# Kernel optimization log

Measured on AMD Instinct MI355X. Metric: run time of the kernel, lower is better.

The kernel has to match this reference:

```python
import jax, jax.numpy as jnp
import numpy as np

N_NODES = 50000
N_EDGES = 800000


def gat_conv(x, src, dst, ea, W, We, a_s, a_d, a_e, b, n_nodes):
    """PyG GATConv with edge_dim, add_self_loops=True, fill_value='mean', concat=True."""
    H, C = a_s.shape
    dt = x.dtype
    # self-loop edge_attr = mean of incoming edge attrs per destination node
    deg = jax.ops.segment_sum(jnp.ones((src.shape[0],), dt), dst, num_segments=n_nodes)
    loop_attr = jax.ops.segment_sum(ea, dst, num_segments=n_nodes) / jnp.clip(deg, 1.0)[:, None]
    nodes = jnp.arange(n_nodes, dtype=src.dtype)
    s = jnp.concatenate([src, nodes])
    d = jnp.concatenate([dst, nodes])
    e_attr = jnp.concatenate([ea, loop_attr], axis=0)       # [E2, edge_dim]
    h = (x @ W).reshape(n_nodes, H, C)                       # [N,H,C]
    e = (e_attr @ We).reshape(-1, H, C)                      # [E2,H,C]
    a_src = jnp.einsum('nhc,hc->nh', h, a_s)                 # [N,H]
    a_dst = jnp.einsum('nhc,hc->nh', h, a_d)
    a_edg = jnp.einsum('ehc,hc->eh', e, a_e)                 # [E2,H]
    lg = jax.nn.leaky_relu(a_src[s] + a_dst[d] + a_edg, 0.2)  # [E2,H]
    m = jax.ops.segment_max(lg, d, num_segments=n_nodes)     # every node has a self-loop
    p = jnp.exp(lg - m[d])
    z = jax.ops.segment_sum(p, d, num_segments=n_nodes)
    alpha = p / z[d]                                         # segment softmax over dst
    out = jax.ops.segment_sum(alpha[:, :, None] * h[s], d, num_segments=n_nodes)
    return out.reshape(n_nodes, H * C) + b


def setup_inputs() -> dict:
    key = jax.random.key(0)
    ks = iter(jax.random.split(key, 40))
    sc = 0.05
    inp = {
        'x': jax.random.normal(next(ks), (N_NODES, 128), jnp.float32),
        'edge_index': jax.random.randint(next(ks), (2, N_EDGES), 0, N_NODES, dtype=jnp.int32),
        'edge_attr': jax.random.uniform(next(ks), (N_EDGES, 1), jnp.float32),
        'fa_w': jax.random.normal(next(ks), (128, 128)) * sc, 'fa_b': jnp.zeros((128,)),
        'W1': jax.random.normal(next(ks), (128, 256)) * sc, 'We1': jax.random.normal(next(ks), (1, 256)) * sc,
        'as1': jax.random.normal(next(ks), (4, 64)) * sc, 'ad1': jax.random.normal(next(ks), (4, 64)) * sc,
        'ae1': jax.random.normal(next(ks), (4, 64)) * sc, 'b1': jnp.zeros((256,)),
        'W2': jax.random.normal(next(ks), (256, 256)) * sc, 'We2': jax.random.normal(next(ks), (1, 256)) * sc,
        'as2': jax.random.normal(next(ks), (4, 64)) * sc, 'ad2': jax.random.normal(next(ks), (4, 64)) * sc,
        'ae2': jax.random.normal(next(ks), (4, 64)) * sc, 'b2': jnp.zeros((256,)),
        'W3': jax.random.normal(next(ks), (256, 64)) * sc, 'We3': jax.random.normal(next(ks), (1, 64)) * sc,
        'as3': jax.random.normal(next(ks), (1, 64)) * sc, 'ad3': jax.random.normal(next(ks), (1, 64)) * sc,
        'ae3': jax.random.normal(next(ks), (1, 64)) * sc, 'b3': jnp.zeros((64,)),
        'r1_w': jax.random.normal(next(ks), (128, 256)) * sc, 'r1_b': jnp.zeros((256,)),
        'r2_w': jax.random.normal(next(ks), (256, 256)) * sc, 'r2_b': jnp.zeros((256,)),
        'ffn_w1': jax.random.normal(next(ks), (128, 64)) * sc, 'ffn_b1': jnp.zeros((64,)),
        'ffn_w2': jax.random.normal(next(ks), (64, 64)) * sc, 'ffn_b2': jnp.zeros((64,)),
    }
    return inp


def reference(x, edge_index, edge_attr, fa_w, fa_b,
              W1, We1, as1, ad1, ae1, b1,
              W2, We2, as2, ad2, ae2, b2,
              W3, We3, as3, ad3, ae3, b3,
              r1_w, r1_b, r2_w, r2_b,
              ffn_w1, ffn_b1, ffn_w2, ffn_b2):
    n = x.shape[0]
    src, dst = edge_index[0], edge_index[1]
    # feature attention gate
    x = x * jax.nn.sigmoid(x @ fa_w + fa_b)
    xr1 = x @ r1_w + r1_b
    z1 = gat_conv(x, src, dst, edge_attr, W1, We1, as1, ad1, ae1, b1, n)
    z1 = jax.nn.leaky_relu(z1, 0.01) + xr1          # dropout = identity (eval)
    z2 = gat_conv(z1, src, dst, edge_attr, W2, We2, as2, ad2, ae2, b2, n)
    z2 = jax.nn.leaky_relu(z2, 0.01) + (z1 @ r2_w + r2_b)
    z3 = gat_conv(z2, src, dst, edge_attr, W3, We3, as3, ad3, ae3, b3, n)
    z_self = jax.nn.relu(x @ ffn_w1 + ffn_b1) @ ffn_w2 + ffn_b2
    z3 = jax.nn.leaky_relu(z3, 0.01) + z_self
    return z3
```

## Files before the change

### kernel.cpp

```cpp
#include <hip/hip_runtime.h>
#include <hip/hip_bf16.h>


typedef unsigned short u16;
typedef unsigned int   u32;
typedef __attribute__((ext_vector_type(8))) short short8;
typedef __attribute__((ext_vector_type(4))) float float4v;

typedef const __attribute__((address_space(1))) u32* gptr_t;
typedef __attribute__((address_space(3))) u32* lptr_t;
#define GLOAD_LDS16(g, l) \
    __builtin_amdgcn_global_load_lds((gptr_t)(const void*)(g), (lptr_t)(void*)(l), 16, 0, 0)

static __device__ __forceinline__ u16 f2b(float f) {
    u32 u = __float_as_uint(f);
    u32 r = u + 0x7fffu + ((u >> 16) & 1u);
    return (u16)(r >> 16);
}
static __device__ __forceinline__ float b2f(u16 u) {
    return __uint_as_float(((u32)u) << 16);
}
static __device__ __forceinline__ float lo2f(u32 v) { return __uint_as_float(v << 16); }
static __device__ __forceinline__ float hi2f(u32 v) { return __uint_as_float(v & 0xffff0000u); }
static __device__ __forceinline__ float lrelu02(float x) { return fmaxf(x, 0.2f * x); }

__global__ void prep_mega(const float* __restrict__ x, u16* __restrict__ xb, int n4,
                          const float* s0, const float* s1, const float* s2,
                          const float* s3, const float* s4, const float* s5,
                          const float* s6, const float* s7,
                          u16* d0, u16* d1, u16* d2, u16* d3,
                          u16* d4, u16* d5, u16* d6, u16* d7,
                          const float* We1, const float* ae1,
                          const float* We2, const float* ae2,
                          const float* We3, const float* ae3, float* ce_g,
                          const int* __restrict__ ei,
                          u32* deg, u32* rank, int E) {
    int role = blockIdx.y;
    if (role == 0) {
        int i = blockIdx.x * 256 + threadIdx.x;
        if (i >= n4) return;
        float4 v = ((const float4*)x)[i];
        ushort4 o;
        o.x = f2b(v.x); o.y = f2b(v.y); o.z = f2b(v.z); o.w = f2b(v.w);
        ((ushort4*)xb)[i] = o;
    } else if (role == 2) {
        int e = blockIdx.x * 256 + threadIdx.x;
        if (e >= E) return;
        int d = ei[E + e];
        rank[e] = atomicAdd(&deg[d], 1u);
    } else {
        int wid = blockIdx.x >> 4, sub = blockIdx.x & 15;
        if (wid > 8) return;
        if (wid == 8) {
            if (sub == 0) {
                int t = threadIdx.x;
                if (t < 9) {
                    const float* W; const float* a; int h;
                    if (t < 4)      { W = We1; a = ae1; h = t; }
                    else if (t < 8) { W = We2; a = ae2; h = t - 4; }
                    else            { W = We3; a = ae3; h = 0; }
                    float s = 0.f;
                    for (int c = 0; c < 64; c++) s += W[h * 64 + c] * a[h * 64 + c];
                    ce_g[t] = s;
                }
            }
            return;
        }
        const float* src; u16* dst; int K, N;
        switch (wid) {
            case 0: src = s0; dst = d0; K = 128; N = 128; break;
            case 1: src = s1; dst = d1; K = 128; N = 256; break;
            case 2: src = s2; dst = d2; K = 128; N = 256; break;
            case 3: src = s3; dst = d3; K = 256; N = 256; break;
            case 4: src = s4; dst = d4; K = 256; N = 256; break;
            case 5: src = s5; dst = d5; K = 256; N = 64;  break;
            case 6: src = s6; dst = d6; K = 128; N = 64;  break;
            default: src = s7; dst = d7; K = 64;  N = 64;  break;
        }
        int KN = K * N;
        int nmask = N - 1;
        int nshift = __popc((u32)nmask);
        for (int i = sub * 256 + threadIdx.x; i < KN; i += 16 * 256) {
            int k = i >> nshift, n2 = i & nmask;
            dst[(size_t)n2 * K + k] = f2b(src[i]);
        }
    }
}

__global__ void scan_block_kernel(const u32* __restrict__ deg, int* incl,
                                  int* blocksum, int Nn) {
    __shared__ int sb[256];
    int t = threadIdx.x;
    int n = blockIdx.x * 256 + t;
    int v = (n < Nn) ? (int)deg[n] : 0;
    sb[t] = v;
    __syncthreads();
    for (int off = 1; off < 256; off <<= 1) {
        int x = (t >= off) ? sb[t - off] : 0;
        __syncthreads();
        sb[t] += x;
        __syncthreads();
    }
    if (n < Nn) incl[n] = sb[t];
    if (t == 255) blocksum[blockIdx.x] = sb[255];
}

__global__ void scan_final_kernel(const u32* __restrict__ deg, const int* __restrict__ incl,
                                  const int* __restrict__ blocksum,
                                  int* row_ptr, int Nn) {
    __shared__ int sb[256];
    int t = threadIdx.x;
    int b = blockIdx.x;
    sb[t] = (t < b) ? blocksum[t] : 0;
    __syncthreads();
    for (int off = 128; off > 0; off >>= 1) {
        if (t < off) sb[t] += sb[t + off];
        __syncthreads();
    }
    int base = sb[0];
    int n = b * 256 + t;
    if (n >= Nn) return;
    int d = (int)deg[n];
    int excl = base + incl[n] - d;
    row_ptr[n] = excl;
    if (n == Nn - 1) row_ptr[Nn] = excl + d;
}

__global__ void scatter_kernel(const int* __restrict__ ei, const float* __restrict__ ea,
                               const int* __restrict__ row_ptr, const u32* __restrict__ rank,
                               int2* __restrict__ csr2, int E) {
    int e = blockIdx.x * 256 + threadIdx.x;
    if (e >= E) return;
    int d = ei[E + e];
    int pos = row_ptr[d] + (int)rank[e];
    csr2[pos] = make_int2(ei[e], __float_as_int(ea[e]));
}

template <int EPI, int K>
__global__ __launch_bounds__(256)
void gemm128_kernel(const u16* __restrict__ A, const u16* __restrict__ Bt,
                    const float* __restrict__ bias,
                    float* __restrict__ Cf, u16* __restrict__ Cb, int N) {
    __shared__ u16 As[128 * 32];
    __shared__ u16 Bs[128 * 32];
    int t = threadIdx.x;
    int w = t >> 6, lane = t & 63;
    int wm = w & 1, wn = w >> 1;
    int lm = lane & 15, q = lane >> 4;
    int bm = blockIdx.x * 128, bn = blockIdx.y * 128;

    float4v acc[4][4];
#pragma unroll
    for (int i = 0; i < 4; i++)
#pragma unroll
        for (int j = 0; j < 4; j++) acc[i][j] = (float4v){0.f, 0.f, 0.f, 0.f};

    int srow = lane >> 2;
    int scol = (lane & 3) * 8;
    const u16* aG = A + (size_t)(bm + w * 32 + srow) * K + scol;
    const u16* bG = Bt + (size_t)(bn + w * 32 + srow) * K + scol;
    u16* aL0 = &As[(w * 32) * 32];
    u16* aL1 = &As[(w * 32 + 16) * 32];
    u16* bL0 = &Bs[(w * 32) * 32];
    u16* bL1 = &Bs[(w * 32 + 16) * 32];

#pragma unroll
    for (int k0 = 0; k0 < K; k0 += 32) {
        GLOAD_LDS16(aG + k0, aL0);
        GLOAD_LDS16(aG + (size_t)16 * K + k0, aL1);
        GLOAD_LDS16(bG + k0, bL0);
        GLOAD_LDS16(bG + (size_t)16 * K + k0, bL1);
        __syncthreads();

        short8 af[4], bf[4];
#pragma unroll
        for (int i = 0; i < 4; i++)
            af[i] = *(const short8*)&As[(64 * wm + 16 * i + lm) * 32 + q * 8];
#pragma unroll
        for (int j = 0; j < 4; j++)
            bf[j] = *(const short8*)&Bs[(64 * wn + 16 * j + lm) * 32 + q * 8];
#pragma unroll
        for (int i = 0; i < 4; i++)
#pragma unroll
            for (int j = 0; j < 4; j++)
                acc[i][j] = __builtin_amdgcn_mfma_f32_16x16x32_bf16(af[i], bf[j], acc[i][j], 0, 0, 0);
        __syncthreads();
    }

#pragma unroll
    for (int i = 0; i < 4; i++)
#pragma unroll
        for (int j = 0; j < 4; j++) {
            int col = bn + 64 * wn + 16 * j + lm;
#pragma unroll
            for (int r = 0; r < 4; r++) {
                int row = bm + 64 * wm + 16 * i + q * 4 + r;
                float v = acc[i][j][r];
                if (EPI == 4) {
                    if (col < 256) {
                        v += bias[col];
                        Cf[(size_t)row * 256 + col] = v;
                    } else {
                        Cb[(size_t)row * 256 + (col - 256)] = f2b(v);
                    }
                } else {
                    Cb[(size_t)row * N + col] = f2b(v);
                }
            }
        }
}

template <int EPI, int K>
__global__ __launch_bounds__(256)
void gemm_kernel(const u16* __restrict__ A, const u16* __restrict__ Bt,
                 const float* __restrict__ bias, const u16* __restrict__ extraB,
                 float* __restrict__ Cf, u16* __restrict__ Cb, int N) {
#define LDSS 40
    __shared__ u16 As[64 * LDSS];
    __shared__ u16 Bs[64 * LDSS];
    int t = threadIdx.x;
    int bm = blockIdx.x * 64, bn = blockIdx.y * 64;
    int w = t >> 6, lane = t & 63;
    int wm = w & 1, wn = w >> 1;
    int lm = lane & 15, q = lane >> 4;

    float4v acc[2][2];
#pragma unroll
    for (int i = 0; i < 2; i++)
#pragma unroll
        for (int j = 0; j < 2; j++) acc[i][j] = (float4v){0.f, 0.f, 0.f, 0.f};

    int ar = t >> 2;
    int ac = (t & 3) * 8;
    const u16* aPtr = A + (size_t)(bm + ar) * K + ac;
    const u16* bPtr = Bt + (size_t)(bn + ar) * K + ac;

#pragma unroll
    for (int k0 = 0; k0 < K; k0 += 32) {
        uint4 av = *(const uint4*)(aPtr + k0);
        uint4 bv = *(const uint4*)(bPtr + k0);
        *(uint4*)&As[ar * LDSS + ac] = av;
        *(uint4*)&Bs[ar * LDSS + ac] = bv;
        __syncthreads();

        short8 fa0 = *(const short8*)&As[(32 * wm + lm) * LDSS + q * 8];
        short8 fa1 = *(const short8*)&As[(32 * wm + 16 + lm) * LDSS + q * 8];
        short8 fb0 = *(const short8*)&Bs[(32 * wn + lm) * LDSS + q * 8];
        short8 fb1 = *(const short8*)&Bs[(32 * wn + 16 + lm) * LDSS + q * 8];
        acc[0][0] = __builtin_amdgcn_mfma_f32_16x16x32_bf16(fa0, fb0, acc[0][0], 0, 0, 0);
        acc[0][1] = __builtin_amdgcn_mfma_f32_16x16x32_bf16(fa0, fb1, acc[0][1], 0, 0, 0);
        acc[1][0] = __builtin_amdgcn_mfma_f32_16x16x32_bf16(fa1, fb0, acc[1][0], 0, 0, 0);
        acc[1][1] = __builtin_amdgcn_mfma_f32_16x16x32_bf16(fa1, fb1, acc[1][1], 0, 0, 0);
        __syncthreads();
    }

#pragma unroll
    for (int i = 0; i < 2; i++)
#pragma unroll
        for (int j = 0; j < 2; j++) {
            int col = bn + 32 * wn + 16 * j + lm;
            float bval = (EPI >= 1) ? bias[col] : 0.f;
#pragma unroll
            for (int r = 0; r < 4; r++) {
                int row = bm + 32 * wm + 16 * i + q * 4 + r;
                float v = acc[i][j][r] + bval;
                if (EPI == 2) v = fmaxf(v, 0.f);
                if (EPI == 3) {
                    float xv = b2f(extraB[(size_t)row * N + col]);
                    v = xv / (1.f + __expf(-v));
                }
                size_t o = (size_t)row * N + col;
                if (EPI == 1) Cf[o] = v;
                else Cb[o] = f2b(v);
            }
        }
}

__global__ __launch_bounds__(256)
void att4_kernel(const uint2* __restrict__ hb2, const float* __restrict__ a_s,
                 const float* __restrict__ a_d, float* att_s, float* att_d, int Nn) {
    int wv = threadIdx.x >> 6;
    int n = blockIdx.x * 4 + wv;
    if (n >= Nn) return;
    int lane = threadIdx.x & 63;
    float4 as4 = *(const float4*)&a_s[lane * 4];
    float4 ad4 = *(const float4*)&a_d[lane * 4];
    uint2 v = hb2[(size_t)n * 64 + lane];
    float c0 = lo2f(v.x), c1 = hi2f(v.x), c2 = lo2f(v.y), c3 = hi2f(v.y);
    float ps = c0 * as4.x + c1 * as4.y + c2 * as4.z + c3 * as4.w;
    float pd = c0 * ad4.x + c1 * ad4.y + c2 * ad4.z + c3 * ad4.w;
#pragma unroll
    for (int off = 8; off > 0; off >>= 1) {
        ps += __shfl_down(ps, off);
        pd += __shfl_down(pd, off);
    }
    if ((lane & 15) == 0) {
        att_s[n * 4 + (lane >> 4)] = ps;
        att_d[n * 4 + (lane >> 4)] = pd;
    }
}

__global__ __launch_bounds__(256)
void att1_kernel(const u32* __restrict__ hb, const float* __restrict__ a_s,
                 const float* __restrict__ a_d, float* att_s, float* att_d, int Nn) {
    int wv = threadIdx.x >> 6;
    int n = blockIdx.x * 4 + wv;
    if (n >= Nn) return;
    int lane = threadIdx.x & 63;
    int cl = lane & 31;
    float2 as2 = *(const float2*)&a_s[cl * 2];
    float2 ad2 = *(const float2*)&a_d[cl * 2];
    u32 v = hb[(u32)n * 32u + cl];
    float c0 = lo2f(v), c1 = hi2f(v);
    float ps = c0 * as2.x + c1 * as2.y;
    float pd = c0 * ad2.x + c1 * ad2.y;
    if (lane >= 32) { ps = 0.f; pd = 0.f; }
#pragma unroll
    for (int off = 16; off > 0; off >>= 1) {
        ps += __shfl_down(ps, off);
        pd += __shfl_down(pd, off);
    }
    if (lane == 0) {
        att_s[n] = ps;
        att_d[n] = pd;
    }
}

__global__ __launch_bounds__(256)
void agg4_kernel(const uint2* __restrict__ hb2,
                 const float* __restrict__ att_s, const float* __restrict__ att_d,
                 const int* __restrict__ row_ptr, const int2* __restrict__ csr2,
                 const float* __restrict__ ce_g, const float* __restrict__ bias,
                 const float* __restrict__ resid, u16* __restrict__ outb, int Nn) {
    int wv = __builtin_amdgcn_readfirstlane(threadIdx.x >> 6);
    int n = blockIdx.x * 4 + wv;
    if (n >= Nn) return;
    int lane = threadIdx.x & 63;
    int hh = lane >> 4;

    float ce = ce_g[hh];
    float adn = att_d[n * 4 + hh];
    float asn = att_s[n * 4 + hh];
    uint2 sv = hb2[(size_t)n * 64 + lane];
    float z = 0.f, qsum = 0.f;
    float aA0 = 0.f, aA1 = 0.f, aA2 = 0.f, aA3 = 0.f;
    float aB0 = 0.f, aB1 = 0.f, aB2 = 0.f, aB3 = 0.f;

    int e0 = row_ptr[n], e1 = row_ptr[n + 1];
    for (int base = e0; base < e1; base += 64) {
        int cnt = min(64, e1 - base);
        int2 cc = csr2[base + min(lane, cnt - 1)];
        int vsrc = cc.x;
        float vea = __int_as_float(cc.y);
        int i = 0;
        for (; i + 8 <= cnt; i += 8) {
            int s0 = __shfl(vsrc, i),     s1 = __shfl(vsrc, i + 1);
            int s2 = __shfl(vsrc, i + 2), s3 = __shfl(vsrc, i + 3);
            int s4 = __shfl(vsrc, i + 4), s5 = __shfl(vsrc, i + 5);
            int s6 = __shfl(vsrc, i + 6), s7 = __shfl(vsrc, i + 7);
            float q0 = __shfl(vea, i),     q1 = __shfl(vea, i + 1);
            float q2 = __shfl(vea, i + 2), q3 = __shfl(vea, i + 3);
            float q4 = __shfl(vea, i + 4), q5 = __shfl(vea, i + 5);
            float q6 = __shfl(vea, i + 6), q7 = __shfl(vea, i + 7);
            float g0 = att_s[(u32)s0 * 4u + hh], g1 = att_s[(u32)s1 * 4u + hh];
            float g2 = att_s[(u32)s2 * 4u + hh], g3 = att_s[(u32)s3 * 4u + hh];
            float g4 = att_s[(u32)s4 * 4u + hh], g5 = att_s[(u32)s5 * 4u + hh];
            float g6 = att_s[(u32)s6 * 4u + hh], g7 = att_s[(u32)s7 * 4u + hh];
            uint2 v0 = hb2[(u32)s0 * 64u + lane], v1 = hb2[(u32)s1 * 64u + lane];
            uint2 v2 = hb2[(u32)s2 * 64u + lane], v3 = hb2[(u32)s3 * 64u + lane];
            uint2 v4 = hb2[(u32)s4 * 64u + lane], v5 = hb2[(u32)s5 * 64u + lane];
            uint2 v6 = hb2[(u32)s6 * 64u + lane], v7 = hb2[(u32)s7 * 64u + lane];
            float p0 = __expf(lrelu02(g0 + adn + q0 * ce));
            float p1 = __expf(lrelu02(g1 + adn + q1 * ce));
            float p2 = __expf(lrelu02(g2 + adn + q2 * ce));
            float p3 = __expf(lrelu02(g3 + adn + q3 * ce));
            float p4 = __expf(lrelu02(g4 + adn + q4 * ce));
            float p5 = __expf(lrelu02(g5 + adn + q5 * ce));
            float p6 = __expf(lrelu02(g6 + adn + q6 * ce));
            float p7 = __expf(lrelu02(g7 + adn + q7 * ce));
            qsum += ((q0 + q1) + (q2 + q3)) + ((q4 + q5) + (q6 + q7));
            z += ((p0 + p1) + (p2 + p3)) + ((p4 + p5) + (p6 + p7));
            aA0 = fmaf(p0, lo2f(v0.x), aA0); aA1 = fmaf(p0, hi2f(v0.x), aA1);
            aA2 = fmaf(p0, lo2f(v0.y), aA2); aA3 = fmaf(p0, hi2f(v0.y), aA3);
            aB0 = fmaf(p1, lo2f(v1.x), aB0); aB1 = fmaf(p1, hi2f(v1.x), aB1);
            aB2 = fmaf(p1, lo2f(v1.y), aB2); aB3 = fmaf(p1, hi2f(v1.y), aB3);
            aA0 = fmaf(p2, lo2f(v2.x), aA0); aA1 = fmaf(p2, hi2f(v2.x), aA1);
            aA2 = fmaf(p2, lo2f(v2.y), aA2); aA3 = fmaf(p2, hi2f(v2.y), aA3);
            aB0 = fmaf(p3, lo2f(v3.x), aB0); aB1 = fmaf(p3, hi2f(v3.x), aB1);
            aB2 = fmaf(p3, lo2f(v3.y), aB2); aB3 = fmaf(p3, hi2f(v3.y), aB3);
            aA0 = fmaf(p4, lo2f(v4.x), aA0); aA1 = fmaf(p4, hi2f(v4.x), aA1);
            aA2 = fmaf(p4, lo2f(v4.y), aA2); aA3 = fmaf(p4, hi2f(v4.y), aA3);
            aB0 = fmaf(p5, lo2f(v5.x), aB0); aB1 = fmaf(p5, hi2f(v5.x), aB1);
            aB2 = fmaf(p5, lo2f(v5.y), aB2); aB3 = fmaf(p5, hi2f(v5.y), aB3);
            aA0 = fmaf(p6, lo2f(v6.x), aA0); aA1 = fmaf(p6, hi2f(v6.x), aA1);
            aA2 = fmaf(p6, lo2f(v6.y), aA2); aA3 = fmaf(p6, hi2f(v6.y), aA3);
            aB0 = fmaf(p7, lo2f(v7.x), aB0); aB1 = fmaf(p7, hi2f(v7.x), aB1);
            aB2 = fmaf(p7, lo2f(v7.y), aB2); aB3 = fmaf(p7, hi2f(v7.y), aB3);
        }
        for (; i < cnt; i++) {
            int s = __shfl(vsrc, i);
            float q = __shfl(vea, i);
            float g = att_s[(u32)s * 4u + hh];
            uint2 v = hb2[(u32)s * 64u + lane];
            float p = __expf(lrelu02(g + adn + q * ce));
            qsum += q;
            z += p;
            aA0 = fmaf(p, lo2f(v.x), aA0); aA1 = fmaf(p, hi2f(v.x), aA1);
            aA2 = fmaf(p, lo2f(v.y), aA2); aA3 = fmaf(p, hi2f(v.y), aA3);
        }
    }
    float la = qsum / (float)max(e1 - e0, 1);
    float ps = __expf(lrelu02(asn + adn + la * ce));
    z += ps;
    float a0 = aA0 + aB0 + ps * lo2f(sv.x);
    float a1 = aA1 + aB1 + ps * hi2f(sv.x);
    float a2 = aA2 + aB2 + ps * lo2f(sv.y);
    float a3 = aA3 + aB3 + ps * hi2f(sv.y);

    float inv = 1.f / z;
    int c0 = lane * 4;
    float4 bv = *(const float4*)&bias[c0];
    float4 rv = *(const float4*)&resid[(size_t)n * 256 + c0];
    float o0 = fmaf(a0, inv, bv.x);
    float o1 = fmaf(a1, inv, bv.y);
    float o2 = fmaf(a2, inv, bv.z);
    float o3 = fmaf(a3, inv, bv.w);
    o0 = fmaxf(o0, 0.01f * o0) + rv.x;
    o1 = fmaxf(o1, 0.01f * o1) + rv.y;
    o2 = fmaxf(o2, 0.01f * o2) + rv.z;
    o3 = fmaxf(o3, 0.01f * o3) + rv.w;
    uint2 packed;
    packed.x = ((u32)f2b(o0)) | (((u32)f2b(o1)) << 16);
    packed.y = ((u32)f2b(o2)) | (((u32)f2b(o3)) << 16);
    ((uint2*)outb)[(size_t)n * 64 + lane] = packed;
}

__global__ __launch_bounds__(256)
void agg1_kernel(const uint2* __restrict__ hb2,
                 const float* __restrict__ att_s, const float* __restrict__ att_d,
                 const int* __restrict__ row_ptr, const int2* __restrict__ csr2,
                 const float* __restrict__ ce_g, const float* __restrict__ bias,
                 const float* __restrict__ resid, float* __restrict__ outf, int Nn) {
    int wv = __builtin_amdgcn_readfirstlane(threadIdx.x >> 6);
    int n = blockIdx.x * 4 + wv;
    if (n >= Nn) return;
    int lane = threadIdx.x & 63;
    int qtr = lane >> 4;
    int cl = lane & 15;

    float ce = ce_g[8];
    float adn = att_d[n];
    float asn = att_s[n];
    uint2 sv = hb2[(u32)n * 16u + cl];
    float z = 0.f, qsum = 0.f;
    float a0 = 0.f, a1 = 0.f, a2 = 0.f, a3 = 0.f;

    int e0 = row_ptr[n], e1 = row_ptr[n + 1];
    for (int base = e0; base < e1; base += 64) {
        int cnt = min(64, e1 - base);
        int2 cc = csr2[base + min(lane, cnt - 1)];
        int vsrc = cc.x;
        float vea = __int_as_float(cc.y);
        for (int i = 0; i < cnt; i += 4) {
            int idx = min(i + qtr, cnt - 1);
            int s = __shfl(vsrc, idx);
            float q = __shfl(vea, idx);
            bool act = (i + qtr < cnt);
            float p = __expf(lrelu02(att_s[s] + adn + q * ce));
            p = act ? p : 0.f;
            q = act ? q : 0.f;
            uint2 v = hb2[(u32)s * 16u + cl];
            z += p;
            qsum += q;
            a0 = fmaf(p, lo2f(v.x), a0);
            a1 = fmaf(p, hi2f(v.x), a1);
            a2 = fmaf(p, lo2f(v.y), a2);
            a3 = fmaf(p, hi2f(v.y), a3);
        }
    }
    z += __shfl_xor(z, 16);      z += __shfl_xor(z, 32);
    qsum += __shfl_xor(qsum, 16); qsum += __shfl_xor(qsum, 32);
    a0 += __shfl_xor(a0, 16);    a0 += __shfl_xor(a0, 32);
    a1 += __shfl_xor(a1, 16);    a1 += __shfl_xor(a1, 32);
    a2 += __shfl_xor(a2, 16);    a2 += __shfl_xor(a2, 32);
    a3 += __shfl_xor(a3, 16);    a3 += __shfl_xor(a3, 32);

    float la = qsum / (float)max(e1 - e0, 1);
    float ps = __expf(lrelu02(asn + adn + la * ce));
    z += ps;
    a0 += ps * lo2f(sv.x);
    a1 += ps * hi2f(sv.x);
    a2 += ps * lo2f(sv.y);
    a3 += ps * hi2f(sv.y);

    if (lane < 16) {
        float inv = 1.f / z;
        int c0 = cl * 4;
        float4 bv = *(const float4*)&bias[c0];
        float4 rv = *(const float4*)&resid[(size_t)n * 64 + c0];
        float o0 = fmaf(a0, inv, bv.x);
        float o1 = fmaf(a1, inv, bv.y);
        float o2 = fmaf(a2, inv, bv.z);
        float o3 = fmaf(a3, inv, bv.w);
        o0 = fmaxf(o0, 0.01f * o0) + rv.x;
        o1 = fmaxf(o1, 0.01f * o1) + rv.y;
        o2 = fmaxf(o2, 0.01f * o2) + rv.z;
        o3 = fmaxf(o3, 0.01f * o3) + rv.w;
        *(float4*)&outf[(size_t)n * 64 + c0] = make_float4(o0, o1, o2, o3);
    }
}

extern "C" void kernel_launch(void* const* d_in, const int* in_sizes, int n_in,
                              void* d_out, int out_size, void* d_ws, size_t ws_size,
                              hipStream_t stream) {
    const float* x    = (const float*)d_in[0];
    const int*   ei   = (const int*)d_in[1];
    const float* ea   = (const float*)d_in[2];
    const float* fa_w = (const float*)d_in[3];
    const float* fa_b = (const float*)d_in[4];
    const float* W1   = (const float*)d_in[5];
    const float* We1  = (const float*)d_in[6];
    const float* as1  = (const float*)d_in[7];
    const float* ad1  = (const float*)d_in[8];
    const float* ae1  = (const float*)d_in[9];
    const float* b1   = (const float*)d_in[10];
    const float* W2   = (const float*)d_in[11];
    const float* We2  = (const float*)d_in[12];
    const float* as2  = (const float*)d_in[13];
    const float* ad2  = (const float*)d_in[14];
    const float* ae2  = (const float*)d_in[15];
    const float* b2   = (const float*)d_in[16];
    const float* W3   = (const float*)d_in[17];
    const float* We3  = (const float*)d_in[18];
    const float* as3  = (const float*)d_in[19];
    const float* ad3  = (const float*)d_in[20];
    const float* ae3  = (const float*)d_in[21];
    const float* b3   = (const float*)d_in[22];
    const float* r1_w = (const float*)d_in[23];
    const float* r1_b = (const float*)d_in[24];
    const float* r2_w = (const float*)d_in[25];
    const float* r2_b = (const float*)d_in[26];
    const float* fw1  = (const float*)d_in[27];
    const float* fb1  = (const float*)d_in[28];
    const float* fw2  = (const float*)d_in[29];
    const float* fb2  = (const float*)d_in[30];

    const int Nn = in_sizes[0] / 128;
    const int E  = in_sizes[1] / 2;

    char* ws = (char*)d_ws;
    size_t off = 0;
    auto alloc = [&](size_t bytes) -> char* {
        char* p = ws + off;
        off += (bytes + 255) & ~((size_t)255);
        return p;
    };
    u32*   deg      = (u32*)alloc((size_t)Nn * 4);
    u32*   rank     = (u32*)alloc((size_t)E * 4);
    int*   incl     = (int*)alloc((size_t)Nn * 4);
    int*   row_ptr  = (int*)alloc((size_t)(Nn + 1) * 4);
    int*   blocksum = (int*)alloc(1024);
    float* att_s    = (float*)alloc((size_t)Nn * 16);
    float* att_d    = (float*)alloc((size_t)Nn * 16);
    int2*  csr2     = (int2*)alloc((size_t)E * 8);
    float* ce_g     = (float*)alloc(64);
    u16* xbf   = (u16*)alloc((size_t)(Nn + 128) * 128 * 2);
    u16* xg_bf = (u16*)alloc((size_t)(Nn + 128) * 128 * 2);
    u16* h_bf  = (u16*)alloc((size_t)(Nn + 128) * 256 * 2);
    u16* z_bf  = (u16*)alloc((size_t)(Nn + 128) * 256 * 2);
    u16* mid_bf = (u16*)alloc((size_t)(Nn + 128) * 64 * 2);
    u16* h3_bf  = (u16*)alloc((size_t)(Nn + 128) * 64 * 2);
    u16* wt_fa = (u16*)alloc(16384 * 2);
    u16* wt_c1 = (u16*)alloc((size_t)512 * 128 * 2);
    u16* wt_c2 = (u16*)alloc((size_t)512 * 256 * 2);
    u16* wt_W3 = (u16*)alloc(16384 * 2);
    u16* wt_f1 = (u16*)alloc(8192 * 2);
    u16* wt_f2 = (u16*)alloc(4096 * 2);
    float* residB = (float*)alloc((size_t)(Nn + 128) * 256 * 4);
    float* zself  = (float*)alloc((size_t)(Nn + 128) * 64 * 4);

    hipMemsetAsync(deg, 0, (size_t)Nn * 4, stream);

    int eb = (E + 255) / 256;
    int nb = (Nn + 255) / 256;
    int n4 = Nn * 128 / 4;
    int xb4 = (n4 + 255) / 256;

    prep_mega<<<dim3(max(xb4, eb), 3), 256, 0, stream>>>(
        x, xbf, n4,
        fa_w, r1_w, W1, r2_w, W2, W3, fw1, fw2,
        wt_fa, wt_c1, wt_c1 + (size_t)256 * 128, wt_c2, wt_c2 + (size_t)256 * 256,
        wt_W3, wt_f1, wt_f2, We1, ae1, We2, ae2, We3, ae3, ce_g,
        ei, deg, rank, E);
    scan_block_kernel<<<nb, 256, 0, stream>>>(deg, incl, blocksum, Nn);
    scan_final_kernel<<<nb, 256, 0, stream>>>(deg, incl, blocksum, row_ptr, Nn);
    scatter_kernel<<<eb, 256, 0, stream>>>(ei, ea, row_ptr, rank, csr2, E);

    int mb  = (Nn + 63) / 64;
    int mb1 = (Nn + 127) / 128;
    int ab  = (Nn + 3) / 4;

    gemm_kernel<3, 128><<<dim3(mb, 2), 256, 0, stream>>>(xbf, wt_fa, fa_b, xbf, nullptr, xg_bf, 128);
    gemm128_kernel<4, 128><<<dim3(mb1, 4), 256, 0, stream>>>(xg_bf, wt_c1, r1_b, residB, h_bf, 512);
    att4_kernel<<<ab, 256, 0, stream>>>((const uint2*)h_bf, as1, ad1, att_s, att_d, Nn);
    agg4_kernel<<<ab, 256, 0, stream>>>((const uint2*)h_bf, att_s, att_d, row_ptr, csr2,
                                        ce_g, b1, residB, z_bf, Nn);
    gemm128_kernel<4, 256><<<dim3(mb1, 4), 256, 0, stream>>>(z_bf, wt_c2, r2_b, residB, h_bf, 512);
    att4_kernel<<<ab, 256, 0, stream>>>((const uint2*)h_bf, as2, ad2, att_s, att_d, Nn);
    agg4_kernel<<<ab, 256, 0, stream>>>((const uint2*)h_bf, att_s, att_d, row_ptr, csr2,
                                        ce_g + 4, b2, residB, z_bf, Nn);
    gemm_kernel<2, 128><<<dim3(mb, 1), 256, 0, stream>>>(xg_bf, wt_f1, fb1, nullptr, nullptr, mid_bf, 64);
    gemm_kernel<1, 64><<<dim3(mb, 1), 256, 0, stream>>>(mid_bf, wt_f2, fb2, nullptr, zself, nullptr, 64);
    gemm_kernel<0, 256><<<dim3(mb, 1), 256, 0, stream>>>(z_bf, wt_W3, nullptr, nullptr, nullptr, h3_bf, 64);
    att1_kernel<<<ab, 256, 0, stream>>>((const u32*)h3_bf, as3, ad3, att_s, att_d, Nn);
    agg1_kernel<<<ab, 256, 0, stream>>>((const uint2*)h3_bf, att_s, att_d, row_ptr, csr2,
                                        ce_g, b3, zself, (float*)d_out, Nn);
}
```

Measured before the change: 490.3 us.

## Fuse FFN first layer into conv1 GEMM, store residuals in bf16, unroll agg by 4

Appends the ffn_w1 weights as an extra 128-column tile to the first combined GEMM, so the ReLU FFN hidden layer is written from its epilogue and its separate launch goes away. Residual and z_self buffers become bf16 instead of fp32, halving their write and read traffic in the GEMM epilogues and aggregation kernels. The agg4 gather loop is unrolled by 4 instead of 8, which lowers register pressure but exposes less memory-level parallelism. The bf16 residuals add rounding error, and the fifth GEMM column tile computes 64 columns that are discarded.

```diff
diff --git a/kernel.cpp b/kernel.cpp
--- a/kernel.cpp
+++ b/kernel.cpp
@@ -139,8 +139,8 @@
 template <int EPI, int K>
 __global__ __launch_bounds__(256)
 void gemm128_kernel(const u16* __restrict__ A, const u16* __restrict__ Bt,
-                    const float* __restrict__ bias,
-                    float* __restrict__ Cf, u16* __restrict__ Cb, int N) {
+                    const float* __restrict__ bias1, const float* __restrict__ bias2,
+                    u16* __restrict__ Cres, u16* __restrict__ Ch, u16* __restrict__ Cmid) {
     __shared__ u16 As[128 * 32];
     __shared__ u16 Bs[128 * 32];
     int t = threadIdx.x;
@@ -196,15 +196,12 @@
             for (int r = 0; r < 4; r++) {
                 int row = bm + 64 * wm + 16 * i + q * 4 + r;
                 float v = acc[i][j][r];
-                if (EPI == 4) {
-                    if (col < 256) {
-                        v += bias[col];
-                        Cf[(size_t)row * 256 + col] = v;
-                    } else {
-                        Cb[(size_t)row * 256 + (col - 256)] = f2b(v);
-                    }
-                } else {
-                    Cb[(size_t)row * N + col] = f2b(v);
+                if (col < 256) {
+                    Cres[(size_t)row * 256 + col] = f2b(v + bias1[col]);
+                } else if (EPI == 4 || col < 512) {
+                    Ch[(size_t)row * 256 + (col - 256)] = f2b(v);
+                } else if (col < 576) {
+                    Cmid[(size_t)row * 64 + (col - 512)] = f2b(fmaxf(v + bias2[col - 512], 0.f));
                 }
             }
         }
@@ -214,7 +211,7 @@
 __global__ __launch_bounds__(256)
 void gemm_kernel(const u16* __restrict__ A, const u16* __restrict__ Bt,
                  const float* __restrict__ bias, const u16* __restrict__ extraB,
-                 float* __restrict__ Cf, u16* __restrict__ Cb, int N) {
+                 u16* __restrict__ Cb, int N) {
 #define LDSS 40
     __shared__ u16 As[64 * LDSS];
     __shared__ u16 Bs[64 * LDSS];
@@ -264,14 +261,11 @@
             for (int r = 0; r < 4; r++) {
                 int row = bm + 32 * wm + 16 * i + q * 4 + r;
                 float v = acc[i][j][r] + bval;
-                if (EPI == 2) v = fmaxf(v, 0.f);
                 if (EPI == 3) {
                     float xv = b2f(extraB[(size_t)row * N + col]);
                     v = xv / (1.f + __expf(-v));
                 }
-                size_t o = (size_t)row * N + col;
-                if (EPI == 1) Cf[o] = v;
-                else Cb[o] = f2b(v);
+                Cb[(size_t)row * N + col] = f2b(v);
             }
         }
 }
@@ -331,7 +325,7 @@
                  const float* __restrict__ att_s, const float* __restrict__ att_d,
                  const int* __restrict__ row_ptr, const int2* __restrict__ csr2,
                  const float* __restrict__ ce_g, const float* __restrict__ bias,
-                 const float* __restrict__ resid, u16* __restrict__ outb, int Nn) {
+                 const uint2* __restrict__ resid2, u16* __restrict__ outb, int Nn) {
     int wv = __builtin_amdgcn_readfirstlane(threadIdx.x >> 6);
     int n = blockIdx.x * 4 + wv;
     if (n >= Nn) return;
@@ -353,49 +347,29 @@
         int vsrc = cc.x;
         float vea = __int_as_float(cc.y);
         int i = 0;
-        for (; i + 8 <= cnt; i += 8) {
-            int s0 = __shfl(vsrc, i),     s1 = __shfl(vsrc, i + 1);
-            int s2 = __shfl(vsrc, i + 2), s3 = __shfl(vsrc, i + 3);
-            int s4 = __shfl(vsrc, i + 4), s5 = __shfl(vsrc, i + 5);
-            int s6 = __shfl(vsrc, i + 6), s7 = __shfl(vsrc, i + 7);
-            float q0 = __shfl(vea, i),     q1 = __shfl(vea, i + 1);
-            float q2 = __shfl(vea, i + 2), q3 = __shfl(vea, i + 3);
-            float q4 = __shfl(vea, i + 4), q5 = __shfl(vea, i + 5);
-            float q6 = __shfl(vea, i + 6), q7 = __shfl(vea, i + 7);
-            float g0 = att_s[(u32)s0 * 4u + hh], g1 = att_s[(u32)s1 * 4u + hh];
-            float g2 = att_s[(u32)s2 * 4u + hh], g3 = att_s[(u32)s3 * 4u + hh];
-            float g4 = att_s[(u32)s4 * 4u + hh], g5 = att_s[(u32)s5 * 4u + hh];
-            float g6 = att_s[(u32)s6 * 4u + hh], g7 = att_s[(u32)s7 * 4u + hh];
-            uint2 v0 = hb2[(u32)s0 * 64u + lane], v1 = hb2[(u32)s1 * 64u + lane];
-            uint2 v2 = hb2[(u32)s2 * 64u + lane], v3 = hb2[(u32)s3 * 64u + lane];
-            uint2 v4 = hb2[(u32)s4 * 64u + lane], v5 = hb2[(u32)s5 * 64u + lane];
-            uint2 v6 = hb2[(u32)s6 * 64u + lane], v7 = hb2[(u32)s7 * 64u + lane];
-            float p0 = __expf(lrelu02(g0 + adn + q0 * ce));
-            float p1 = __expf(lrelu02(g1 + adn + q1 * ce));
-            float p2 = __expf(lrelu02(g2 + adn + q2 * ce));
-            float p3 = __expf(lrelu02(g3 + adn + q3 * ce));
-            float p4 = __expf(lrelu02(g4 + adn + q4 * ce));
-            float p5 = __expf(lrelu02(g5 + adn + q5 * ce));
-            float p6 = __expf(lrelu02(g6 + adn + q6 * ce));
-            float p7 = __expf(lrelu02(g7 + adn + q7 * ce));
-            qsum += ((q0 + q1) + (q2 + q3)) + ((q4 + q5) + (q6 + q7));
-            z += ((p0 + p1) + (p2 + p3)) + ((p4 + p5) + (p6 + p7));
-            aA0 = fmaf(p0, lo2f(v0.x), aA0); aA1 = fmaf(p0, hi2f(v0.x), aA1);
-            aA2 = fmaf(p0, lo2f(v0.y), aA2); aA3 = fmaf(p0, hi2f(v0.y), aA3);
-            aB0 = fmaf(p1, lo2f(v1.x), aB0); aB1 = fmaf(p1, hi2f(v1.x), aB1);
-            aB2 = fmaf(p1, lo2f(v1.y), aB2); aB3 = fmaf(p1, hi2f(v1.y), aB3);
-            aA0 = fmaf(p2, lo2f(v2.x), aA0); aA1 = fmaf(p2, hi2f(v2.x), aA1);
-            aA2 = fmaf(p2, lo2f(v2.y), aA2); aA3 = fmaf(p2, hi2f(v2.y), aA3);
-            aB0 = fmaf(p3, lo2f(v3.x), aB0); aB1 = fmaf(p3, hi2f(v3.x), aB1);
-            aB2 = fmaf(p3, lo2f(v3.y), aB2); aB3 = fmaf(p3, hi2f(v3.y), aB3);
-            aA0 = fmaf(p4, lo2f(v4.x), aA0); aA1 = fmaf(p4, hi2f(v4.x), aA1);
-            aA2 = fmaf(p4, lo2f(v4.y), aA2); aA3 = fmaf(p4, hi2f(v4.y), aA3);
-            aB0 = fmaf(p5, lo2f(v5.x), aB0); aB1 = fmaf(p5, hi2f(v5.x), aB1);
-            aB2 = fmaf(p5, lo2f(v5.y), aB2); aB3 = fmaf(p5, hi2f(v5.y), aB3);
-            aA0 = fmaf(p6, lo2f(v6.x), aA0); aA1 = fmaf(p6, hi2f(v6.x), aA1);
-            aA2 = fmaf(p6, lo2f(v6.y), aA2); aA3 = fmaf(p6, hi2f(v6.y), aA3);
-            aB0 = fmaf(p7, lo2f(v7.x), aB0); aB1 = fmaf(p7, hi2f(v7.x), aB1);
-            aB2 = fmaf(p7, lo2f(v7.y), aB2); aB3 = fmaf(p7, hi2f(v7.y), aB3);
+        for (; i + 4 <= cnt; i += 4) {
+            int sA = __shfl(vsrc, i),     sB = __shfl(vsrc, i + 1);
+            int sC = __shfl(vsrc, i + 2), sD = __shfl(vsrc, i + 3);
+            float qA = __shfl(vea, i),     qB = __shfl(vea, i + 1);
+            float qC = __shfl(vea, i + 2), qD = __shfl(vea, i + 3);
+            float gA = att_s[(u32)sA * 4u + hh], gB = att_s[(u32)sB * 4u + hh];
+            float gC = att_s[(u32)sC * 4u + hh], gD = att_s[(u32)sD * 4u + hh];
+            uint2 vA = hb2[(u32)sA * 64u + lane], vB = hb2[(u32)sB * 64u + lane];
+            uint2 vC = hb2[(u32)sC * 64u + lane], vD = hb2[(u32)sD * 64u + lane];
+            float pA = __expf(lrelu02(gA + adn + qA * ce));
+            float pB = __expf(lrelu02(gB + adn + qB * ce));
+            float pC = __expf(lrelu02(gC + adn + qC * ce));
+            float pD = __expf(lrelu02(gD + adn + qD * ce));
+            qsum += (qA + qB) + (qC + qD);
+            z += (pA + pB) + (pC + pD);
+            aA0 = fmaf(pA, lo2f(vA.x), aA0); aA1 = fmaf(pA, hi2f(vA.x), aA1);
+            aA2 = fmaf(pA, lo2f(vA.y), aA2); aA3 = fmaf(pA, hi2f(vA.y), aA3);
+            aB0 = fmaf(pB, lo2f(vB.x), aB0); aB1 = fmaf(pB, hi2f(vB.x), aB1);
+            aB2 = fmaf(pB, lo2f(vB.y), aB2); aB3 = fmaf(pB, hi2f(vB.y), aB3);
+            aA0 = fmaf(pC, lo2f(vC.x), aA0); aA1 = fmaf(pC, hi2f(vC.x), aA1);
+            aA2 = fmaf(pC, lo2f(vC.y), aA2); aA3 = fmaf(pC, hi2f(vC.y), aA3);
+            aB0 = fmaf(pD, lo2f(vD.x), aB0); aB1 = fmaf(pD, hi2f(vD.x), aB1);
+            aB2 = fmaf(pD, lo2f(vD.y), aB2); aB3 = fmaf(pD, hi2f(vD.y), aB3);
         }
         for (; i < cnt; i++) {
             int s = __shfl(vsrc, i);
@@ -420,15 +394,15 @@
     float inv = 1.f / z;
     int c0 = lane * 4;
     float4 bv = *(const float4*)&bias[c0];
-    float4 rv = *(const float4*)&resid[(size_t)n * 256 + c0];
+    uint2 rr = resid2[(size_t)n * 64 + lane];
     float o0 = fmaf(a0, inv, bv.x);
     float o1 = fmaf(a1, inv, bv.y);
     float o2 = fmaf(a2, inv, bv.z);
     float o3 = fmaf(a3, inv, bv.w);
-    o0 = fmaxf(o0, 0.01f * o0) + rv.x;
-    o1 = fmaxf(o1, 0.01f * o1) + rv.y;
-    o2 = fmaxf(o2, 0.01f * o2) + rv.z;
-    o3 = fmaxf(o3, 0.01f * o3) + rv.w;
+    o0 = fmaxf(o0, 0.01f * o0) + lo2f(rr.x);
+    o1 = fmaxf(o1, 0.01f * o1) + hi2f(rr.x);
+    o2 = fmaxf(o2, 0.01f * o2) + lo2f(rr.y);
+    o3 = fmaxf(o3, 0.01f * o3) + hi2f(rr.y);
     uint2 packed;
     packed.x = ((u32)f2b(o0)) | (((u32)f2b(o1)) << 16);
     packed.y = ((u32)f2b(o2)) | (((u32)f2b(o3)) << 16);
@@ -440,7 +414,7 @@
                  const float* __restrict__ att_s, const float* __restrict__ att_d,
                  const int* __restrict__ row_ptr, const int2* __restrict__ csr2,
                  const float* __restrict__ ce_g, const float* __restrict__ bias,
-                 const float* __restrict__ resid, float* __restrict__ outf, int Nn) {
+                 const uint2* __restrict__ zs2, float* __restrict__ outf, int Nn) {
     int wv = __builtin_amdgcn_readfirstlane(threadIdx.x >> 6);
     int n = blockIdx.x * 4 + wv;
     if (n >= Nn) return;
@@ -478,12 +452,12 @@
             a3 = fmaf(p, hi2f(v.y), a3);
         }
     }
-    z += __shfl_xor(z, 16);      z += __shfl_xor(z, 32);
+    z += __shfl_xor(z, 16);       z += __shfl_xor(z, 32);
     qsum += __shfl_xor(qsum, 16); qsum += __shfl_xor(qsum, 32);
-    a0 += __shfl_xor(a0, 16);    a0 += __shfl_xor(a0, 32);
-    a1 += __shfl_xor(a1, 16);    a1 += __shfl_xor(a1, 32);
-    a2 += __shfl_xor(a2, 16);    a2 += __shfl_xor(a2, 32);
-    a3 += __shfl_xor(a3, 16);    a3 += __shfl_xor(a3, 32);
+    a0 += __shfl_xor(a0, 16);     a0 += __shfl_xor(a0, 32);
+    a1 += __shfl_xor(a1, 16);     a1 += __shfl_xor(a1, 32);
+    a2 += __shfl_xor(a2, 16);     a2 += __shfl_xor(a2, 32);
+    a3 += __shfl_xor(a3, 16);     a3 += __shfl_xor(a3, 32);
 
     float la = qsum / (float)max(e1 - e0, 1);
     float ps = __expf(lrelu02(asn + adn + la * ce));
@@ -497,15 +471,15 @@
         float inv = 1.f / z;
         int c0 = cl * 4;
         float4 bv = *(const float4*)&bias[c0];
-        float4 rv = *(const float4*)&resid[(size_t)n * 64 + c0];
+        uint2 zz = zs2[(u32)n * 16u + cl];
         float o0 = fmaf(a0, inv, bv.x);
         float o1 = fmaf(a1, inv, bv.y);
         float o2 = fmaf(a2, inv, bv.z);
         float o3 = fmaf(a3, inv, bv.w);
-        o0 = fmaxf(o0, 0.01f * o0) + rv.x;
-        o1 = fmaxf(o1, 0.01f * o1) + rv.y;
-        o2 = fmaxf(o2, 0.01f * o2) + rv.z;
-        o3 = fmaxf(o3, 0.01f * o3) + rv.w;
+        o0 = fmaxf(o0, 0.01f * o0) + lo2f(zz.x);
+        o1 = fmaxf(o1, 0.01f * o1) + hi2f(zz.x);
+        o2 = fmaxf(o2, 0.01f * o2) + lo2f(zz.y);
+        o3 = fmaxf(o3, 0.01f * o3) + hi2f(zz.y);
         *(float4*)&outf[(size_t)n * 64 + c0] = make_float4(o0, o1, o2, o3);
     }
 }
@@ -571,13 +545,12 @@
     u16* mid_bf = (u16*)alloc((size_t)(Nn + 128) * 64 * 2);
     u16* h3_bf  = (u16*)alloc((size_t)(Nn + 128) * 64 * 2);
     u16* wt_fa = (u16*)alloc(16384 * 2);
-    u16* wt_c1 = (u16*)alloc((size_t)512 * 128 * 2);
+    u16* wt_c1 = (u16*)alloc((size_t)640 * 128 * 2);
     u16* wt_c2 = (u16*)alloc((size_t)512 * 256 * 2);
     u16* wt_W3 = (u16*)alloc(16384 * 2);
-    u16* wt_f1 = (u16*)alloc(8192 * 2);
     u16* wt_f2 = (u16*)alloc(4096 * 2);
-    float* residB = (float*)alloc((size_t)(Nn + 128) * 256 * 4);
-    float* zself  = (float*)alloc((size_t)(Nn + 128) * 64 * 4);
+    u16* residB = (u16*)alloc((size_t)(Nn + 128) * 256 * 2);
+    u16* zself  = (u16*)alloc((size_t)(Nn + 128) * 64 * 2);
 
     hipMemsetAsync(deg, 0, (size_t)Nn * 4, stream);
 
@@ -590,7 +563,7 @@
         x, xbf, n4,
         fa_w, r1_w, W1, r2_w, W2, W3, fw1, fw2,
         wt_fa, wt_c1, wt_c1 + (size_t)256 * 128, wt_c2, wt_c2 + (size_t)256 * 256,
-        wt_W3, wt_f1, wt_f2, We1, ae1, We2, ae2, We3, ae3, ce_g,
+        wt_W3, wt_c1 + (size_t)512 * 128, wt_f2, We1, ae1, We2, ae2, We3, ae3, ce_g,
         ei, deg, rank, E);
     scan_block_kernel<<<nb, 256, 0, stream>>>(deg, incl, blocksum, Nn);
     scan_final_kernel<<<nb, 256, 0, stream>>>(deg, incl, blocksum, row_ptr, Nn);
@@ -600,19 +573,20 @@
     int mb1 = (Nn + 127) / 128;
     int ab  = (Nn + 3) / 4;
 
-    gemm_kernel<3, 128><<<dim3(mb, 2), 256, 0, stream>>>(xbf, wt_fa, fa_b, xbf, nullptr, xg_bf, 128);
-    gemm128_kernel<4, 128><<<dim3(mb1, 4), 256, 0, stream>>>(xg_bf, wt_c1, r1_b, residB, h_bf, 512);
+    gemm_kernel<3, 128><<<dim3(mb, 2), 256, 0, stream>>>(xbf, wt_fa, fa_b, xbf, xg_bf, 128);
+    gemm128_kernel<6, 128><<<dim3(mb1, 5), 256, 0, stream>>>(xg_bf, wt_c1, r1_b, fb1,
+                                                             residB, h_bf, mid_bf);
     att4_kernel<<<ab, 256, 0, stream>>>((const uint2*)h_bf, as1, ad1, att_s, att_d, Nn);
     agg4_kernel<<<ab, 256, 0, stream>>>((const uint2*)h_bf, att_s, att_d, row_ptr, csr2,
-                                        ce_g, b1, residB, z_bf, Nn);
-    gemm128_kernel<4, 256><<<dim3(mb1, 4), 256, 0, stream>>>(z_bf, wt_c2, r2_b, residB, h_bf, 512);
+                                        ce_g, b1, (const uint2*)residB, z_bf, Nn);
+    gemm128_kernel<4, 256><<<dim3(mb1, 4), 256, 0, stream>>>(z_bf, wt_c2, r2_b, nullptr,
+                                                             residB, h_bf, nullptr);
     att4_kernel<<<ab, 256, 0, stream>>>((const uint2*)h_bf, as2, ad2, att_s, att_d, Nn);
     agg4_kernel<<<ab, 256, 0, stream>>>((const uint2*)h_bf, att_s, att_d, row_ptr, csr2,
-                                        ce_g + 4, b2, residB, z_bf, Nn);
-    gemm_kernel<2, 128><<<dim3(mb, 1), 256, 0, stream>>>(xg_bf, wt_f1, fb1, nullptr, nullptr, mid_bf, 64);
-    gemm_kernel<1, 64><<<dim3(mb, 1), 256, 0, stream>>>(mid_bf, wt_f2, fb2, nullptr, zself, nullptr, 64);
-    gemm_kernel<0, 256><<<dim3(mb, 1), 256, 0, stream>>>(z_bf, wt_W3, nullptr, nullptr, nullptr, h3_bf, 64);
+                                        ce_g + 4, b2, (const uint2*)residB, z_bf, Nn);
+    gemm_kernel<1, 64><<<dim3(mb, 1), 256, 0, stream>>>(mid_bf, wt_f2, fb2, nullptr, zself, 64);
+    gemm_kernel<0, 256><<<dim3(mb, 1), 256, 0, stream>>>(z_bf, wt_W3, nullptr, nullptr, h3_bf, 64);
     att1_kernel<<<ab, 256, 0, stream>>>((const u32*)h3_bf, as3, ad3, att_s, att_d, Nn);
     agg1_kernel<<<ab, 256, 0, stream>>>((const uint2*)h3_bf, att_s, att_d, row_ptr, csr2,
-                                        ce_g, b3, zself, (float*)d_out, Nn);
-}
+                                        ce_g, b3, (const uint2*)zself, (float*)d_out, Nn);
+}
```

New measurement: 494.8 us. Within noise of the previous version (+0.9%).
